# Kernel optimization log

Hardware: AMD Instinct MI355X
Metric: run time of the kernel (lower is better)

## Reference

```python
import jax, jax.numpy as jnp
import numpy as np

IN_DIM = 128; OUT_DIM = 128; H = 8; DK = OUT_DIM // H
N_A = 100000; N_B = 100000; E0 = 400000; E1 = 400000
NUM_TYPES = 2; NUM_REL = 2
EPS = 1e-9; LN_EPS = 1e-5


def setup_inputs() -> dict:
    key = jax.random.key(0)
    ks = jax.random.split(key, 16)
    s = 0.02
    xav = float(np.sqrt(6.0 / (DK + DK)))  # xavier_uniform bound for (dk, dk)
    inp = {}
    inp['x_a'] = jax.random.normal(ks[0], (N_A, IN_DIM), jnp.float32)
    inp['x_b'] = jax.random.normal(ks[1], (N_B, IN_DIM), jnp.float32)
    inp['ew0'] = jax.random.uniform(ks[2], (E0,), jnp.float32)
    inp['ew1'] = jax.random.uniform(ks[3], (E1,), jnp.float32)
    inp['src0'] = jax.random.randint(ks[4], (E0,), 0, N_A)
    inp['dst0'] = jax.random.randint(ks[5], (E0,), 0, N_B)
    inp['src1'] = jax.random.randint(ks[6], (E1,), 0, N_B)
    inp['dst1'] = jax.random.randint(ks[7], (E1,), 0, N_A)
    # per-node-type stacked linear params: [type, in, out]
    inp['Wk'] = jax.random.normal(ks[8], (NUM_TYPES, IN_DIM, OUT_DIM), jnp.float32) * s
    inp['bk'] = jnp.zeros((NUM_TYPES, OUT_DIM), jnp.float32)
    inp['Wq'] = jax.random.normal(ks[9], (NUM_TYPES, IN_DIM, OUT_DIM), jnp.float32) * s
    inp['bq'] = jnp.zeros((NUM_TYPES, OUT_DIM), jnp.float32)
    inp['Wv'] = jax.random.normal(ks[10], (NUM_TYPES, IN_DIM, OUT_DIM), jnp.float32) * s
    inp['bv'] = jnp.zeros((NUM_TYPES, OUT_DIM), jnp.float32)
    inp['Wa'] = jax.random.normal(ks[11], (NUM_TYPES, OUT_DIM, OUT_DIM), jnp.float32) * s
    inp['ba'] = jnp.zeros((NUM_TYPES, OUT_DIM), jnp.float32)
    inp['ln_g'] = jnp.ones((NUM_TYPES, OUT_DIM), jnp.float32)
    inp['ln_b'] = jnp.zeros((NUM_TYPES, OUT_DIM), jnp.float32)
    inp['rel_pri'] = jnp.ones((NUM_REL, H), jnp.float32)
    inp['rel_att'] = jax.random.uniform(ks[12], (NUM_REL, H, DK, DK), jnp.float32, -xav, xav)
    inp['rel_msg'] = jax.random.uniform(ks[13], (NUM_REL, H, DK, DK), jnp.float32, -xav, xav)
    inp['skip'] = jnp.ones((NUM_TYPES,), jnp.float32)
    return inp


def _edge_softmax(logits, dst, n_dst):
    # segment softmax over incoming edges of each dst node; logits: (E, H)
    m = jax.ops.segment_max(logits, dst, num_segments=n_dst)
    e = jnp.exp(logits - m[dst])
    s = jax.ops.segment_sum(e, dst, num_segments=n_dst)
    return e / s[dst]


def _relation(x_s, x_d, src, dst, ew, Wk_s, bk_s, Wq_d, bq_d, Wv_s, bv_s,
              ratt, rmsg, rpri, n_dst):
    # per-relation HGT attention -> aggregated dst messages (n_dst, H, DK)
    k = (x_s @ Wk_s + bk_s).reshape(-1, H, DK)
    k = jnp.einsum('nhd,hde->nhe', k, ratt)
    v = (x_s @ Wv_s + bv_s).reshape(-1, H, DK)
    v = jnp.einsum('nhd,hde->nhe', v, rmsg)
    q = (x_d @ Wq_d + bq_d).reshape(-1, H, DK)
    t = jnp.einsum('ehd,ehd->eh', q[dst], k[src])  # edge dot score (E, H)
    # dst-normalized edge weight -> additive log bias
    ew = jnp.clip(ew, 0.0)
    den = jax.ops.segment_sum(ew, dst, num_segments=n_dst)
    ewn = ew / jnp.maximum(den[dst], EPS)
    t = t + jnp.log(ewn + EPS)[:, None]
    t = t * rpri / jnp.sqrt(jnp.float32(DK))
    a = _edge_softmax(t, dst, n_dst)  # (E, H)
    msg = v[src] * a[:, :, None]      # (E, H, DK)
    return jax.ops.segment_sum(msg, dst, num_segments=n_dst)


def _forward(x_a, x_b, ew0, ew1, Wk, bk, Wq, bq, Wv, bv, Wa, ba, ln_g, ln_b,
             rel_pri, rel_att, rel_msg, skip, src0, dst0, src1, dst1):
    # relation 0: a -> b (src type 0, dst type 1); relation 1: b -> a
    t_b = _relation(x_a, x_b, src0, dst0, ew0, Wk[0], bk[0], Wq[1], bq[1],
                    Wv[0], bv[0], rel_att[0], rel_msg[0], rel_pri[0], x_b.shape[0])
    t_a = _relation(x_b, x_a, src1, dst1, ew1, Wk[1], bk[1], Wq[0], bq[0],
                    Wv[1], bv[1], rel_att[1], rel_msg[1], rel_pri[1], x_a.shape[0])
    def combine(t, base, nid):
        alpha = jax.nn.sigmoid(skip[nid])
        trans = t.reshape(-1, OUT_DIM) @ Wa[nid] + ba[nid]  # dropout: eval mode
        out = trans * alpha + base * (1.0 - alpha)
        mu = jnp.mean(out, axis=-1, keepdims=True)
        var = jnp.var(out, axis=-1, keepdims=True)
        return (out - mu) / jnp.sqrt(var + LN_EPS) * ln_g[nid] + ln_b[nid]
    return combine(t_a, x_a, 0), combine(t_b, x_b, 1)


def reference(x_a, x_b, ew0, ew1, src0, dst0, src1, dst1, Wk, bk, Wq, bq, Wv, bv,
              Wa, ba, ln_g, ln_b, rel_pri, rel_att, rel_msg, skip):
    return _forward(x_a, x_b, ew0, ew1, Wk, bk, Wq, bq, Wv, bv, Wa, ba, ln_g, ln_b,
                    rel_pri, rel_att, rel_msg, skip, src0, dst0, src1, dst1)
```

## Files before the change

kernel.cpp:

```cpp
#include <hip/hip_runtime.h>
#include <cstdint>
#include <cstddef>

#define EPSF 1e-9f

typedef __bf16 bf16x8 __attribute__((ext_vector_type(8)));
typedef float fvec4 __attribute__((ext_vector_type(4)));

__device__ __forceinline__ float blo(unsigned int u) { return __uint_as_float(u << 16); }
__device__ __forceinline__ float bhi(unsigned int u) { return __uint_as_float(u & 0xffff0000u); }
__device__ __forceinline__ unsigned short f2bf(float f) {
  unsigned int u = __float_as_uint(f);
  u += 0x7fffu + ((u >> 16) & 1u);
  return (unsigned short)(u >> 16);
}
__device__ __forceinline__ unsigned int pack2bf(float a, float b) {
  return (unsigned int)f2bf(a) | ((unsigned int)f2bf(b) << 16);
}

__global__ __launch_bounds__(256) void fzero(float* __restrict__ p, long n) {
  long i = (long)blockIdx.x * blockDim.x + threadIdx.x;
  long stride = (long)gridDim.x * blockDim.x;
  long n4 = n >> 2;
  float4* p4 = (float4*)p;
  for (long j = i; j < n4; j += stride) p4[j] = make_float4(0.f, 0.f, 0.f, 0.f);
  for (long j = (n4 << 2) + i; j < n; j += stride) p[j] = 0.f;
}

__global__ __launch_bounds__(256) void fuse_w(
    const float* __restrict__ Wk, const float* __restrict__ bk,
    const float* __restrict__ Wv, const float* __restrict__ bv,
    const float* __restrict__ rel_att, const float* __restrict__ rel_msg,
    __bf16* __restrict__ WkvqT, float* __restrict__ bkvq)
{
  int i = blockIdx.x;
  int t = blockIdx.y;
  int c = threadIdx.x;
  int m = c >> 7, cc = c & 127;
  int h = cc >> 4, e = cc & 15;
  const float* R = (m ? rel_msg : rel_att) + t * 2048 + h * 256;
  const float* srcW = (m ? Wv : Wk) + t * 16384;
  const float* srcB = (m ? bv : bk) + t * 128;
  const float* row = (i < 128) ? (srcW + i * 128) : srcB;
  float acc = 0.f;
#pragma unroll
  for (int d = 0; d < 16; ++d) acc = fmaf(row[h * 16 + d], R[d * 16 + e], acc);
  if (i < 128) WkvqT[(size_t)t * 49152 + (size_t)c * 128 + i] = (__bf16)acc;
  else         bkvq[t * 384 + c] = acc;
}

__global__ __launch_bounds__(128) void cvt_wT(
    const float* __restrict__ Wq, const float* __restrict__ bq,
    const float* __restrict__ Wa,
    __bf16* __restrict__ WkvqT, __bf16* __restrict__ WaT,
    float* __restrict__ bkvq)
{
  int k = blockIdx.x, t = blockIdx.y, c = threadIdx.x;
  if (blockIdx.z == 0) {
    WkvqT[(size_t)t * 49152 + (size_t)(256 + c) * 128 + k] = (__bf16)Wq[t * 16384 + k * 128 + c];
    if (k == 0) bkvq[t * 384 + 256 + c] = bq[t * 128 + c];
  } else {
    WaT[(size_t)t * 16384 + (size_t)c * 128 + k] = (__bf16)Wa[t * 16384 + k * 128 + c];
  }
}

__global__ __launch_bounds__(256) void gemm_kvq(
    const float* __restrict__ Aa, int Ma, const float* __restrict__ Ab, int Mb, int nblk_a,
    const __bf16* __restrict__ WTall, const float* __restrict__ ball,
    __bf16* __restrict__ KVa, __bf16* __restrict__ Qa,
    __bf16* __restrict__ KVb, __bf16* __restrict__ Qb)
{
  __shared__ __bf16 As[64 * 128];
  const int tid = threadIdx.x;
  const bool isA = blockIdx.x < (unsigned)nblk_a;
  const int blk = isA ? blockIdx.x : blockIdx.x - nblk_a;
  const float* A = isA ? Aa : Ab;
  const int M = isA ? Ma : Mb;
  const __bf16* WT = WTall + (isA ? 0 : 49152);
  const float* bs = ball + (isA ? 0 : 384);
  __bf16* KV = isA ? KVa : KVb;
  __bf16* Q  = isA ? Qa : Qb;
  const int rowb = blk * 64;

#pragma unroll
  for (int i = 0; i < 4; ++i) {
    int f = tid + i * 256;
    int r = f >> 4, ch = f & 15;
    int gr = rowb + r; gr = gr < M ? gr : M - 1;
    const float4* ap = (const float4*)(A + (size_t)gr * 128 + ch * 8);
    float4 a0 = ap[0], a1 = ap[1];
    bf16x8 v;
    v[0] = (__bf16)a0.x; v[1] = (__bf16)a0.y; v[2] = (__bf16)a0.z; v[3] = (__bf16)a0.w;
    v[4] = (__bf16)a1.x; v[5] = (__bf16)a1.y; v[6] = (__bf16)a1.z; v[7] = (__bf16)a1.w;
    int sw = (ch * 16) ^ ((r & 7) << 4);
    *(bf16x8*)((char*)As + r * 256 + sw) = v;
  }
  __syncthreads();

  const int l = tid & 63, wid = tid >> 6;
  const int l15 = l & 15, l4 = l >> 4;
  const int wm = wid & 1, wn = wid >> 1;

  bf16x8 af[2][4];
#pragma unroll
  for (int m = 0; m < 2; ++m)
#pragma unroll
    for (int ks = 0; ks < 4; ++ks) {
      int r = wm * 32 + m * 16 + l15;
      int off = (ks * 64 + l4 * 16) ^ ((r & 7) << 4);
      af[m][ks] = *(const bf16x8*)((const char*)As + r * 256 + off);
    }

#pragma unroll
  for (int t = 0; t < 3; ++t) {
    const int colb = t * 128 + wn * 64;
    fvec4 z = {0.f, 0.f, 0.f, 0.f};
    fvec4 acc[2][4];
#pragma unroll
    for (int m = 0; m < 2; ++m)
#pragma unroll
      for (int n = 0; n < 4; ++n) acc[m][n] = z;

    bf16x8 bfr[4][4];
#pragma unroll
    for (int n = 0; n < 4; ++n)
#pragma unroll
      for (int ks = 0; ks < 4; ++ks)
        bfr[n][ks] = *(const bf16x8*)(WT + (size_t)(colb + n * 16 + l15) * 128 + ks * 32 + l4 * 8);

#pragma unroll
    for (int ks = 0; ks < 4; ++ks)
#pragma unroll
      for (int m = 0; m < 2; ++m)
#pragma unroll
        for (int n = 0; n < 4; ++n)
          acc[m][n] = __builtin_amdgcn_mfma_f32_16x16x32_bf16(bfr[n][ks], af[m][ks], acc[m][n], 0, 0, 0);

#pragma unroll
    for (int m = 0; m < 2; ++m) {
      int r = rowb + wm * 32 + m * 16 + l15;
      if (r >= M) continue;
#pragma unroll
      for (int n = 0; n < 4; ++n) {
        int cb = colb + n * 16 + l4 * 4;
        fvec4 b4 = *(const fvec4*)(bs + cb);
        uint2 w;
        w.x = pack2bf(acc[m][n][0] + b4[0], acc[m][n][1] + b4[1]);
        w.y = pack2bf(acc[m][n][2] + b4[2], acc[m][n][3] + b4[3]);
        if (t < 2) *(uint2*)(KV + (size_t)r * 256 + cb) = w;
        else       *(uint2*)(Q + (size_t)r * 128 + (cb - 256)) = w;
      }
    }
  }
}

__global__ __launch_bounds__(256) void csr_count2(
    const int* __restrict__ dst0, int E0, const int* __restrict__ dst1, int E1,
    int* __restrict__ deg, int NB)
{
  int e = blockIdx.x * 256 + threadIdx.x;
  if (e < E0) atomicAdd(&deg[dst0[e]], 1);
  else if (e < E0 + E1) atomicAdd(&deg[NB + dst1[e - E0]], 1);
}

__global__ __launch_bounds__(256) void csr_partial(
    const int* __restrict__ deg, int N, int* __restrict__ partial)
{
  int base = blockIdx.x * 1024 + threadIdx.x * 4;
  int s = 0;
#pragma unroll
  for (int i = 0; i < 4; ++i) if (base + i < N) s += deg[base + i];
#pragma unroll
  for (int m = 1; m < 64; m <<= 1) s += __shfl_xor(s, m, 64);
  __shared__ int wsum[4];
  if ((threadIdx.x & 63) == 0) wsum[threadIdx.x >> 6] = s;
  __syncthreads();
  if (threadIdx.x == 0) partial[blockIdx.x] = wsum[0] + wsum[1] + wsum[2] + wsum[3];
}

__global__ void csr_scan_partials(const int* __restrict__ partial,
                                  int* __restrict__ pscan, int NP)
{
  if (blockIdx.x == 0 && threadIdx.x == 0) {
    int s = 0;
    for (int i = 0; i < NP; ++i) { pscan[i] = s; s += partial[i]; }
  }
}

__global__ __launch_bounds__(256) void csr_scan_chunk(
    const int* __restrict__ deg, const int* __restrict__ pscan,
    int* __restrict__ row_start, int* __restrict__ cursor, int N)
{
  __shared__ int ls[256];
  int base = blockIdx.x * 1024 + threadIdx.x * 4;
  int v0 = 0, v1 = 0, v2 = 0, v3 = 0;
  if (base + 0 < N) v0 = deg[base + 0];
  if (base + 1 < N) v1 = deg[base + 1];
  if (base + 2 < N) v2 = deg[base + 2];
  if (base + 3 < N) v3 = deg[base + 3];
  int s = v0 + v1 + v2 + v3;
  ls[threadIdx.x] = s;
  __syncthreads();
  for (int off = 1; off < 256; off <<= 1) {
    int t = (threadIdx.x >= off) ? ls[threadIdx.x - off] : 0;
    __syncthreads();
    ls[threadIdx.x] += t;
    __syncthreads();
  }
  int excl = pscan[blockIdx.x] + ls[threadIdx.x] - s;
  int p0 = excl, p1 = excl + v0, p2 = excl + v0 + v1, p3 = excl + v0 + v1 + v2;
  if (base + 0 < N) { row_start[base + 0] = p0; cursor[base + 0] = p0; }
  if (base + 1 < N) { row_start[base + 1] = p1; cursor[base + 1] = p1; }
  if (base + 2 < N) { row_start[base + 2] = p2; cursor[base + 2] = p2; }
  if (base + 3 < N) { row_start[base + 3] = p3; cursor[base + 3] = p3; }
}

__global__ __launch_bounds__(256) void csr_scatter2(
    const int* __restrict__ dst0, const int* __restrict__ src0, const float* __restrict__ ew0, int E0,
    const int* __restrict__ dst1, const int* __restrict__ src1, const float* __restrict__ ew1, int E1,
    int* __restrict__ cursor, int* __restrict__ sidx, float* __restrict__ ewc, int NB)
{
  int e = blockIdx.x * 256 + threadIdx.x;
  if (e < E0) {
    int p = atomicAdd(&cursor[dst0[e]], 1);
    sidx[p] = src0[e];
    ewc[p] = fmaxf(ew0[e], 0.f);
  } else if (e < E0 + E1) {
    int e1 = e - E0;
    int p = atomicAdd(&cursor[NB + dst1[e1]], 1);
    sidx[p] = src1[e1];
    ewc[p] = fmaxf(ew1[e1], 0.f);
  }
}

__device__ __forceinline__ void proc_edge(
    float qlo, float qhi, unsigned int ku, unsigned int vu, float w,
    float inv_den, float pr, float& s, float2& acc)
{
  float t = qlo * blo(ku) + qhi * bhi(ku);
  t += __shfl_xor(t, 1, 64);
  t += __shfl_xor(t, 2, 64);
  t += __shfl_xor(t, 4, 64);
  float x = __expf((t + __logf(w * inv_den + EPSF)) * pr);
  s += x;
  acc.x = fmaf(x, blo(vu), acc.x);
  acc.y = fmaf(x, bhi(vu), acc.y);
}

__global__ __launch_bounds__(256) void hgt_dst(
    const __bf16* __restrict__ kv0, const __bf16* __restrict__ q0,
    const __bf16* __restrict__ kv1, const __bf16* __restrict__ q1,
    const int* __restrict__ row_start, const int* __restrict__ deg,
    const int* __restrict__ sidx, const float* __restrict__ ewc,
    const float* __restrict__ pri16,
    __bf16* __restrict__ agg0, __bf16* __restrict__ agg1, int NB, int N2)
{
  int n = (blockIdx.x * 256 + threadIdx.x) >> 6;
  int lane = threadIdx.x & 63;
  if (n >= N2) return;
  bool g0 = n < NB;
  int nl = g0 ? n : n - NB;
  const unsigned short* kvs = (const unsigned short*)(g0 ? kv0 : kv1);
  const unsigned short* qrow = (const unsigned short*)(g0 ? q0 : q1) + (size_t)nl * 128;
  const float* pri8 = pri16 + (g0 ? 0 : 8);
  int c0 = lane * 2;
  unsigned int* out = (unsigned int*)((g0 ? agg0 : agg1) + (size_t)nl * 128 + c0);
  int d = deg[n];
  if (d == 0) { out[0] = 0u; return; }
  int base = row_start[n];

  float ds = 0.f;
  for (int j = lane; j < d; j += 64) ds += ewc[base + j];
#pragma unroll
  for (int m = 1; m < 64; m <<= 1) ds += __shfl_xor(ds, m, 64);
  float inv_den = 1.f / fmaxf(ds, EPSF);

  int h = lane >> 3;
  float pr = pri8[h] * 0.25f;
  unsigned int qu = *(const unsigned int*)(qrow + c0);
  float qlo = blo(qu), qhi = bhi(qu);

  float s = 0.f;
  float2 acc = make_float2(0.f, 0.f);
  int j = 0;
  for (; j + 4 <= d; j += 4) {
    int b = base + j;
    int si0 = sidx[b], si1 = sidx[b + 1], si2 = sidx[b + 2], si3 = sidx[b + 3];
    float w0 = ewc[b], w1 = ewc[b + 1], w2 = ewc[b + 2], w3 = ewc[b + 3];
    const unsigned short* p0 = kvs + (size_t)si0 * 256 + c0;
    const unsigned short* p1 = kvs + (size_t)si1 * 256 + c0;
    const unsigned short* p2 = kvs + (size_t)si2 * 256 + c0;
    const unsigned short* p3 = kvs + (size_t)si3 * 256 + c0;
    unsigned int k0 = *(const unsigned int*)p0, v0 = *(const unsigned int*)(p0 + 128);
    unsigned int k1 = *(const unsigned int*)p1, v1 = *(const unsigned int*)(p1 + 128);
    unsigned int k2 = *(const unsigned int*)p2, v2 = *(const unsigned int*)(p2 + 128);
    unsigned int k3 = *(const unsigned int*)p3, v3 = *(const unsigned int*)(p3 + 128);
    proc_edge(qlo, qhi, k0, v0, w0, inv_den, pr, s, acc);
    proc_edge(qlo, qhi, k1, v1, w1, inv_den, pr, s, acc);
    proc_edge(qlo, qhi, k2, v2, w2, inv_den, pr, s, acc);
    proc_edge(qlo, qhi, k3, v3, w3, inv_den, pr, s, acc);
  }
  for (; j < d; ++j) {
    int b = base + j;
    const unsigned short* p = kvs + (size_t)sidx[b] * 256 + c0;
    proc_edge(qlo, qhi, *(const unsigned int*)p, *(const unsigned int*)(p + 128),
              ewc[b], inv_den, pr, s, acc);
  }
  float is = 1.f / s;
  out[0] = pack2bf(acc.x * is, acc.y * is);
}

__global__ __launch_bounds__(256) void wa_ln(
    const __bf16* __restrict__ Ag_a, const __bf16* __restrict__ Ag_b,
    const __bf16* __restrict__ WaT, const float* __restrict__ ba,
    const float* __restrict__ x_a, const float* __restrict__ x_b,
    const float* __restrict__ lng, const float* __restrict__ lnb,
    const float* __restrict__ skip, float* __restrict__ out,
    int NA, int NB, int nblk_a)
{
  const int tid = threadIdx.x, l = tid & 63, wid = tid >> 6;
  const int l15 = l & 15, l4 = l >> 4;
  const bool isA = blockIdx.x < (unsigned)nblk_a;
  const int blk = isA ? blockIdx.x : blockIdx.x - nblk_a;
  const int M = isA ? NA : NB;
  const __bf16* Ag = isA ? Ag_a : Ag_b;
  const __bf16* WT = WaT + (isA ? 0 : 16384);
  const float* bias = ba + (isA ? 0 : 128);
  const float* xb = isA ? x_a : x_b;
  const float* g = lng + (isA ? 0 : 128);
  const float* bb = lnb + (isA ? 0 : 128);
  float* o = out + (isA ? (size_t)0 : (size_t)NA * 128);
  const int rowb = blk * 64 + wid * 16;
  const int r = rowb + l15;
  const int rc = r < M ? r : M - 1;

  bf16x8 af[4];
#pragma unroll
  for (int ks = 0; ks < 4; ++ks)
    af[ks] = *(const bf16x8*)(Ag + (size_t)rc * 128 + ks * 32 + l4 * 8);

  fvec4 z = {0.f, 0.f, 0.f, 0.f};
  fvec4 acc[8];
#pragma unroll
  for (int n = 0; n < 8; ++n) acc[n] = z;
#pragma unroll
  for (int ks = 0; ks < 4; ++ks)
#pragma unroll
    for (int n = 0; n < 8; ++n) {
      bf16x8 wf = *(const bf16x8*)(WT + (size_t)(n * 16 + l15) * 128 + ks * 32 + l4 * 8);
      acc[n] = __builtin_amdgcn_mfma_f32_16x16x32_bf16(wf, af[ks], acc[n], 0, 0, 0);
    }

  float alpha = 1.f / (1.f + __expf(-skip[isA ? 0 : 1]));
  float onema = 1.f - alpha;
  float vals[8][4];
  float psum = 0.f, psq = 0.f;
#pragma unroll
  for (int n = 0; n < 8; ++n) {
    int cb = n * 16 + l4 * 4;
    fvec4 b4 = *(const fvec4*)(bias + cb);
    fvec4 xv = *(const fvec4*)(xb + (size_t)rc * 128 + cb);
#pragma unroll
    for (int reg = 0; reg < 4; ++reg) {
      float v = (acc[n][reg] + b4[reg]) * alpha + xv[reg] * onema;
      vals[n][reg] = v;
      psum += v;
      psq = fmaf(v, v, psq);
    }
  }
  psum += __shfl_xor(psum, 16, 64); psq += __shfl_xor(psq, 16, 64);
  psum += __shfl_xor(psum, 32, 64); psq += __shfl_xor(psq, 32, 64);
  float mu = psum * (1.f / 128.f);
  float var = psq * (1.f / 128.f) - mu * mu;
  float is = 1.f / sqrtf(var + 1e-5f);

  if (r < M) {
#pragma unroll
    for (int n = 0; n < 8; ++n) {
      int cb = n * 16 + l4 * 4;
      fvec4 g4 = *(const fvec4*)(g + cb);
      fvec4 bb4 = *(const fvec4*)(bb + cb);
      fvec4 ov;
#pragma unroll
      for (int reg = 0; reg < 4; ++reg)
        ov[reg] = (vals[n][reg] - mu) * is * g4[reg] + bb4[reg];
      *(fvec4*)(o + (size_t)r * 128 + cb) = ov;
    }
  }
}

extern "C" void kernel_launch(void* const* d_in, const int* in_sizes, int n_in,
                              void* d_out, int out_size, void* d_ws, size_t ws_size,
                              hipStream_t stream)
{
  const float* x_a = (const float*)d_in[0];
  const float* x_b = (const float*)d_in[1];
  const float* ew0 = (const float*)d_in[2];
  const float* ew1 = (const float*)d_in[3];
  const int* src0 = (const int*)d_in[4];
  const int* dst0 = (const int*)d_in[5];
  const int* src1 = (const int*)d_in[6];
  const int* dst1 = (const int*)d_in[7];
  const float* Wk = (const float*)d_in[8];
  const float* bk = (const float*)d_in[9];
  const float* Wq = (const float*)d_in[10];
  const float* bq = (const float*)d_in[11];
  const float* Wv = (const float*)d_in[12];
  const float* bv = (const float*)d_in[13];
  const float* Wa = (const float*)d_in[14];
  const float* ba = (const float*)d_in[15];
  const float* ln_g = (const float*)d_in[16];
  const float* ln_b = (const float*)d_in[17];
  const float* rel_pri = (const float*)d_in[18];
  const float* rel_att = (const float*)d_in[19];
  const float* rel_msg = (const float*)d_in[20];
  const float* skip = (const float*)d_in[21];

  int NA = in_sizes[0] / 128, NB = in_sizes[1] / 128;
  int E0 = in_sizes[2], E1 = in_sizes[3];
  int NMAX = NA > NB ? NA : NB;
  int NM = (NMAX + 255) & ~255;
  int N2 = NA + NB;
  int N2M = (N2 + 255) & ~255;
  int E2 = E0 + E1;
  int E2M = (E2 + 255) & ~255;

  char* wsbase = (char*)d_ws;
  size_t off = 0;
  auto alloc = [&](size_t bytes) { char* p = wsbase + off; off += (bytes + 255) & ~(size_t)255; return p; };
  __bf16* kvb_a = (__bf16*)alloc((size_t)NM * 256 * 2);
  __bf16* kvb_b = (__bf16*)alloc((size_t)NM * 256 * 2);
  __bf16* qd_a  = (__bf16*)alloc((size_t)NM * 128 * 2);
  __bf16* qd_b  = (__bf16*)alloc((size_t)NM * 128 * 2);
  __bf16* agg_a = (__bf16*)alloc((size_t)NM * 128 * 2);
  __bf16* agg_b = (__bf16*)alloc((size_t)NM * 128 * 2);
  __bf16* WkvqT = (__bf16*)alloc(2 * 384 * 128 * 2);
  __bf16* WaT   = (__bf16*)alloc(2 * 128 * 128 * 2);
  float* bkvq   = (float*)alloc(2 * 384 * 4);
  int* deg      = (int*)alloc((size_t)N2M * 4);
  int* row_st   = (int*)alloc((size_t)N2M * 4);
  int* cur      = (int*)alloc((size_t)N2M * 4);
  int* partial  = (int*)alloc(1024 * 4);
  int* pscan    = (int*)alloc(1024 * 4);
  int* sidx     = (int*)alloc((size_t)E2M * 4);
  float* ewc    = (float*)alloc((size_t)E2M * 4);

  float* outf = (float*)d_out;
  dim3 b256(256);
  auto cdiv = [](int a, int b) { return (unsigned)((a + b - 1) / b); };

  fuse_w<<<dim3(129, 2), b256, 0, stream>>>(Wk, bk, Wv, bv, rel_att, rel_msg, WkvqT, bkvq);
  cvt_wT<<<dim3(128, 2, 2), 128, 0, stream>>>(Wq, bq, Wa, WkvqT, WaT, bkvq);

  int NP = (N2 + 1023) / 1024;
  fzero<<<64, b256, 0, stream>>>((float*)deg, N2);
  csr_count2<<<cdiv(E2, 256), b256, 0, stream>>>(dst0, E0, dst1, E1, deg, NB);
  csr_partial<<<NP, b256, 0, stream>>>(deg, N2, partial);
  csr_scan_partials<<<1, 64, 0, stream>>>(partial, pscan, NP);
  csr_scan_chunk<<<NP, b256, 0, stream>>>(deg, pscan, row_st, cur, N2);
  csr_scatter2<<<cdiv(E2, 256), b256, 0, stream>>>(dst0, src0, ew0, E0,
                                                   dst1, src1, ew1, E1,
                                                   cur, sidx, ewc, NB);

  int nba = cdiv(NA, 64), nbb = cdiv(NB, 64);
  gemm_kvq<<<nba + nbb, b256, 0, stream>>>(x_a, NA, x_b, NB, nba, WkvqT, bkvq,
                                           kvb_a, qd_a, kvb_b, qd_b);

  hgt_dst<<<cdiv(N2, 4), b256, 0, stream>>>(kvb_a, qd_b, kvb_b, qd_a,
                                            row_st, deg, sidx, ewc, rel_pri,
                                            agg_b, agg_a, NB, N2);

  wa_ln<<<nba + nbb, b256, 0, stream>>>(agg_a, agg_b, WaT, ba, x_a, x_b,
                                        ln_g, ln_b, skip, outf, NA, NB, nba);
}
```

Measured before the change: 582.8 us.

## Make KVQ projection GEMM persistent with register-prefetched double-buffered A tiles

```diff
diff --git a/kernel.cpp b/kernel.cpp
--- a/kernel.cpp
+++ b/kernel.cpp
@@ -64,91 +64,112 @@
   }
 }
 
-__global__ __launch_bounds__(256) void gemm_kvq(
-    const float* __restrict__ Aa, int Ma, const float* __restrict__ Ab, int Mb, int nblk_a,
+__global__ __launch_bounds__(256, 4) void gemm_kvq(
+    const float* __restrict__ Aa, int Ma, const float* __restrict__ Ab, int Mb,
     const __bf16* __restrict__ WTall, const float* __restrict__ ball,
     __bf16* __restrict__ KVa, __bf16* __restrict__ Qa,
-    __bf16* __restrict__ KVb, __bf16* __restrict__ Qb)
-{
-  __shared__ __bf16 As[64 * 128];
+    __bf16* __restrict__ KVb, __bf16* __restrict__ Qb,
+    int ntile_a, int ntiles)
+{
+  __shared__ __bf16 As[2][64 * 128];
   const int tid = threadIdx.x;
-  const bool isA = blockIdx.x < (unsigned)nblk_a;
-  const int blk = isA ? blockIdx.x : blockIdx.x - nblk_a;
-  const float* A = isA ? Aa : Ab;
-  const int M = isA ? Ma : Mb;
-  const __bf16* WT = WTall + (isA ? 0 : 49152);
-  const float* bs = ball + (isA ? 0 : 384);
-  __bf16* KV = isA ? KVa : KVb;
-  __bf16* Q  = isA ? Qa : Qb;
-  const int rowb = blk * 64;
-
-#pragma unroll
-  for (int i = 0; i < 4; ++i) {
-    int f = tid + i * 256;
-    int r = f >> 4, ch = f & 15;
-    int gr = rowb + r; gr = gr < M ? gr : M - 1;
-    const float4* ap = (const float4*)(A + (size_t)gr * 128 + ch * 8);
-    float4 a0 = ap[0], a1 = ap[1];
-    bf16x8 v;
-    v[0] = (__bf16)a0.x; v[1] = (__bf16)a0.y; v[2] = (__bf16)a0.z; v[3] = (__bf16)a0.w;
-    v[4] = (__bf16)a1.x; v[5] = (__bf16)a1.y; v[6] = (__bf16)a1.z; v[7] = (__bf16)a1.w;
-    int sw = (ch * 16) ^ ((r & 7) << 4);
-    *(bf16x8*)((char*)As + r * 256 + sw) = v;
-  }
-  __syncthreads();
-
   const int l = tid & 63, wid = tid >> 6;
   const int l15 = l & 15, l4 = l >> 4;
   const int wm = wid & 1, wn = wid >> 1;
 
-  bf16x8 af[2][4];
-#pragma unroll
-  for (int m = 0; m < 2; ++m)
-#pragma unroll
-    for (int ks = 0; ks < 4; ++ks) {
-      int r = wm * 32 + m * 16 + l15;
-      int off = (ks * 64 + l4 * 16) ^ ((r & 7) << 4);
-      af[m][ks] = *(const bf16x8*)((const char*)As + r * 256 + off);
-    }
-
-#pragma unroll
-  for (int t = 0; t < 3; ++t) {
-    const int colb = t * 128 + wn * 64;
-    fvec4 z = {0.f, 0.f, 0.f, 0.f};
-    fvec4 acc[2][4];
+  float4 st[8];
+  auto issue = [&](int tile) {
+    const bool isA = tile < ntile_a;
+    const float* A = isA ? Aa : Ab;
+    const int M = isA ? Ma : Mb;
+    const int rowb = (isA ? tile : tile - ntile_a) * 64;
+#pragma unroll
+    for (int i = 0; i < 4; ++i) {
+      int f = tid + i * 256;
+      int r = f >> 4, ch = f & 15;
+      int gr = rowb + r; gr = gr < M ? gr : M - 1;
+      const float4* ap = (const float4*)(A + (size_t)gr * 128 + ch * 8);
+      st[2 * i] = ap[0]; st[2 * i + 1] = ap[1];
+    }
+  };
+
+  int it = blockIdx.x;
+  if (it < ntiles) issue(it);
+  int cur = 0;
+  for (; it < ntiles; it += gridDim.x, cur ^= 1) {
+#pragma unroll
+    for (int i = 0; i < 4; ++i) {
+      int f = tid + i * 256;
+      int r = f >> 4, ch = f & 15;
+      float4 a0 = st[2 * i], a1 = st[2 * i + 1];
+      bf16x8 v;
+      v[0] = (__bf16)a0.x; v[1] = (__bf16)a0.y; v[2] = (__bf16)a0.z; v[3] = (__bf16)a0.w;
+      v[4] = (__bf16)a1.x; v[5] = (__bf16)a1.y; v[6] = (__bf16)a1.z; v[7] = (__bf16)a1.w;
+      int sw = (ch * 16) ^ ((r & 7) << 4);
+      *(bf16x8*)((char*)As[cur] + r * 256 + sw) = v;
+    }
+    __syncthreads();
+
+    int nxt = it + gridDim.x;
+    if (nxt < ntiles) issue(nxt);
+
+    const bool isA = it < ntile_a;
+    const int M = isA ? Ma : Mb;
+    const int rowb = (isA ? it : it - ntile_a) * 64;
+    const __bf16* WT = WTall + (isA ? 0 : 49152);
+    const float* bs = ball + (isA ? 0 : 384);
+    __bf16* KV = isA ? KVa : KVb;
+    __bf16* Q  = isA ? Qa : Qb;
+
+    bf16x8 af[2][4];
 #pragma unroll
     for (int m = 0; m < 2; ++m)
 #pragma unroll
-      for (int n = 0; n < 4; ++n) acc[m][n] = z;
-
-    bf16x8 bfr[4][4];
-#pragma unroll
-    for (int n = 0; n < 4; ++n)
+      for (int ks = 0; ks < 4; ++ks) {
+        int r = wm * 32 + m * 16 + l15;
+        int off = (ks * 64 + l4 * 16) ^ ((r & 7) << 4);
+        af[m][ks] = *(const bf16x8*)((const char*)As[cur] + r * 256 + off);
+      }
+
+#pragma unroll
+    for (int t = 0; t < 3; ++t) {
+      const int colb = t * 128 + wn * 64;
+      fvec4 z = {0.f, 0.f, 0.f, 0.f};
+      fvec4 acc[2][4];
+#pragma unroll
+      for (int m = 0; m < 2; ++m)
+#pragma unroll
+        for (int n = 0; n < 4; ++n) acc[m][n] = z;
+
+      bf16x8 bfr[4][4];
+#pragma unroll
+      for (int n = 0; n < 4; ++n)
+#pragma unroll
+        for (int ks = 0; ks < 4; ++ks)
+          bfr[n][ks] = *(const bf16x8*)(WT + (size_t)(colb + n * 16 + l15) * 128 + ks * 32 + l4 * 8);
+
 #pragma unroll
       for (int ks = 0; ks < 4; ++ks)
-        bfr[n][ks] = *(const bf16x8*)(WT + (size_t)(colb + n * 16 + l15) * 128 + ks * 32 + l4 * 8);
-
-#pragma unroll
-    for (int ks = 0; ks < 4; ++ks)
-#pragma unroll
-      for (int m = 0; m < 2; ++m)
-#pragma unroll
-        for (int n = 0; n < 4; ++n)
-          acc[m][n] = __builtin_amdgcn_mfma_f32_16x16x32_bf16(bfr[n][ks], af[m][ks], acc[m][n], 0, 0, 0);
-
-#pragma unroll
-    for (int m = 0; m < 2; ++m) {
-      int r = rowb + wm * 32 + m * 16 + l15;
-      if (r >= M) continue;
-#pragma unroll
-      for (int n = 0; n < 4; ++n) {
-        int cb = colb + n * 16 + l4 * 4;
-        fvec4 b4 = *(const fvec4*)(bs + cb);
-        uint2 w;
-        w.x = pack2bf(acc[m][n][0] + b4[0], acc[m][n][1] + b4[1]);
-        w.y = pack2bf(acc[m][n][2] + b4[2], acc[m][n][3] + b4[3]);
-        if (t < 2) *(uint2*)(KV + (size_t)r * 256 + cb) = w;
-        else       *(uint2*)(Q + (size_t)r * 128 + (cb - 256)) = w;
+#pragma unroll
+        for (int m = 0; m < 2; ++m)
+#pragma unroll
+          for (int n = 0; n < 4; ++n)
+            acc[m][n] = __builtin_amdgcn_mfma_f32_16x16x32_bf16(bfr[n][ks], af[m][ks], acc[m][n], 0, 0, 0);
+
+#pragma unroll
+      for (int m = 0; m < 2; ++m) {
+        int r = rowb + wm * 32 + m * 16 + l15;
+        if (r >= M) continue;
+#pragma unroll
+        for (int n = 0; n < 4; ++n) {
+          int cb = colb + n * 16 + l4 * 4;
+          fvec4 b4 = *(const fvec4*)(bs + cb);
+          uint2 w;
+          w.x = pack2bf(acc[m][n][0] + b4[0], acc[m][n][1] + b4[1]);
+          w.y = pack2bf(acc[m][n][2] + b4[2], acc[m][n][3] + b4[3]);
+          if (t < 2) *(uint2*)(KV + (size_t)r * 256 + cb) = w;
+          else       *(uint2*)(Q + (size_t)r * 128 + (cb - 256)) = w;
+        }
       }
     }
   }
@@ -462,14 +483,16 @@
                                                    dst1, src1, ew1, E1,
                                                    cur, sidx, ewc, NB);
 
-  int nba = cdiv(NA, 64), nbb = cdiv(NB, 64);
-  gemm_kvq<<<nba + nbb, b256, 0, stream>>>(x_a, NA, x_b, NB, nba, WkvqT, bkvq,
-                                           kvb_a, qd_a, kvb_b, qd_b);
+  int nta = cdiv(NA, 64), ntb = cdiv(NB, 64);
+  int ntiles = nta + ntb;
+  int ggrid = ntiles < 1024 ? ntiles : 1024;
+  gemm_kvq<<<ggrid, b256, 0, stream>>>(x_a, NA, x_b, NB, WkvqT, bkvq,
+                                       kvb_a, qd_a, kvb_b, qd_b, nta, ntiles);
 
   hgt_dst<<<cdiv(N2, 4), b256, 0, stream>>>(kvb_a, qd_b, kvb_b, qd_a,
                                             row_st, deg, sidx, ewc, rel_pri,
                                             agg_b, agg_a, NB, N2);
 
-  wa_ln<<<nba + nbb, b256, 0, stream>>>(agg_a, agg_b, WaT, ba, x_a, x_b,
-                                        ln_g, ln_b, skip, outf, NA, NB, nba);
-}
+  wa_ln<<<nta + ntb, b256, 0, stream>>>(agg_a, agg_b, WaT, ba, x_a, x_b,
+                                        ln_g, ln_b, skip, outf, NA, NB, nta);
+}
```

New measurement: 628.4 us. +7.8%, slower.
